# Kernel optimization log

Hardware: AMD Instinct MI355X
Metric: run time of the kernel (lower is better)

The kernel has to match this reference:

```python
import jax, jax.numpy as jnp
import numpy as np

CONTACT_THRESH = 0.01
COLLISION_THRESH = 0.005
WEIGHT_PEN = 100.0
WEIGHT_MISS = 10.0
# MANO fingertip + palm contact-zone vertex indices (hardcoded in module)
CONTACT_IDX = np.array([745, 317, 444, 556, 673, 95, 182, 234, 279, 320])

SCALE = 0.1  # place points in a 0.1 m cube so mm-scale thresholds are meaningful


def setup_inputs() -> dict:
    key = jax.random.key(0)
    k1, k2, k3, k4 = jax.random.split(key, 4)
    B, NH, V = 8, 778, 40000
    hand_verts = jax.random.uniform(k1, (B, NH, 3), dtype=jnp.float32) * SCALE
    obj_verts = jax.random.uniform(k2, (B, V, 3), dtype=jnp.float32) * SCALE
    hand_faces = jax.random.randint(k3, (1538, 3), 0, NH, dtype=jnp.int64 if jax.config.read('jax_enable_x64') else jnp.int32)
    obj_faces = jax.random.randint(k4, (79996, 3), 0, V, dtype=jnp.int64 if jax.config.read('jax_enable_x64') else jnp.int32)
    return {"hand_verts": hand_verts, "obj_verts": obj_verts,
            "hand_faces": hand_faces, "obj_faces": obj_faces}


def _min_dists(a, b):
    """Brute-force 1-NN: min Euclidean distance from each point in a [B,N,3] to b [B,M,3] -> [B,N]."""
    a_sq = jnp.sum(a * a, axis=-1, keepdims=True)          # [B,N,1]
    b_sq = jnp.sum(b * b, axis=-1)                          # [B,M]
    ab = jnp.einsum('bnd,bmd->bnm', a, b)                   # [B,N,M]
    d2 = jnp.maximum(a_sq + b_sq[:, None, :] - 2.0 * ab, 0.0)
    return jnp.sqrt(jnp.min(d2, axis=2))                    # [B,N]


def _masked_mean(vals, mask):
    cnt = jnp.sum(mask)
    s = jnp.sum(jnp.where(mask, vals, 0.0))
    return jnp.where(cnt > 0, s / jnp.maximum(cnt, 1).astype(vals.dtype), jnp.zeros((), vals.dtype))


def reference(hand_verts, obj_verts, hand_faces, obj_faces):
    # faces are unused by the loss (as in the torch module)
    idx = jnp.asarray(CONTACT_IDX)
    # distances are computed under no_grad / detached in the original
    dists = jax.lax.stop_gradient(_min_dists(hand_verts, obj_verts))              # [B,778]
    contact_dists = jax.lax.stop_gradient(_min_dists(hand_verts[:, idx, :], obj_verts))  # [B,10]

    pen_mask = dists < COLLISION_THRESH
    pen_loss = _masked_mean((COLLISION_THRESH - dists) ** 2, pen_mask)

    att_mask = (contact_dists > COLLISION_THRESH) & (contact_dists < CONTACT_THRESH)
    att_loss = _masked_mean(contact_dists ** 2, att_mask)

    contact_loss = WEIGHT_PEN * pen_loss + WEIGHT_MISS * att_loss
    dist_mean = jnp.mean(dists)
    num_contacts = jnp.sum(att_mask).astype(jnp.int32)
    num_penetrations = jnp.sum(pen_mask).astype(jnp.int32)
    return (contact_loss, pen_loss, att_loss, dist_mean, num_contacts, num_penetrations)
```

## Files before the change

kernel.cpp:

```cpp
#include <hip/hip_runtime.h>
#include <math.h>

constexpr int NH     = 778;
constexpr int T      = 16;
constexpr int NTILES = (NH + T - 1) / T;
constexpr int NHPAD  = NTILES * T;
constexpr int BLK    = 256;
constexpr int CHUNKP = 2560;
constexpr int LPP    = CHUNKP / BLK;

__global__ __launch_bounds__(256) void transform_kernel(
    const float* __restrict__ hand,
    const float* __restrict__ obj,
    float4* __restrict__ otf,
    float4* __restrict__ htf,
    unsigned int* __restrict__ minb,
    int V, int Vpad, int B)
{
    const int i = blockIdx.x * 256 + threadIdx.x;
    if (i < B * NH) minb[i] = 0x7F7F7F7Fu;
    if (i < B * NHPAD) {
        const int b = i / NHPAD;
        const int h = min(i - b * NHPAD, NH - 1);
        const float* p = hand + ((size_t)b * NH + h) * 3;
        const float x = p[0], y = p[1], z = p[2];
        htf[i] = make_float4(-2.f * x, -2.f * y, -2.f * z,
                             fmaf(x, x, fmaf(y, y, z * z)));
    }
    if (i < B * Vpad) {
        const int b = i / Vpad;
        const int j = i - b * Vpad;
        if (j < V) {
            const float* p = obj + ((size_t)b * V + j) * 3;
            const float x = p[0], y = p[1], z = p[2];
            otf[i] = make_float4(x, y, z, fmaf(x, x, fmaf(y, y, z * z)));
        } else {
            otf[i] = make_float4(0.f, 0.f, 0.f, 3.4e38f);
        }
    }
}

__global__ __launch_bounds__(BLK, 4) void nn_min_kernel(
    const float4* __restrict__ otf,
    const float4* __restrict__ htf,
    unsigned int* __restrict__ minb,
    int Vpad)
{
    const int tile = blockIdx.x;
    const int c    = blockIdx.y;
    const int b    = blockIdx.z;
    const int tid  = threadIdx.x;

    const float4* hp = htf + (size_t)b * NHPAD + tile * T;
    float4 h[T];
#pragma unroll
    for (int t = 0; t < T; ++t) h[t] = hp[t];

    const float4* op = otf + (size_t)b * Vpad + c * CHUNKP + tid;
    float m[T];
#pragma unroll
    for (int t = 0; t < T; ++t) m[t] = 3.4e38f;

#pragma unroll
    for (int k = 0; k < LPP; ++k) {
        const float4 o = op[k * BLK];
#pragma unroll
        for (int t = 0; t < T; ++t) {
            float v = fmaf(h[t].x, o.x, o.w);
            v = fmaf(h[t].y, o.y, v);
            v = fmaf(h[t].z, o.z, v);
            m[t] = fminf(m[t], v);
        }
    }

#pragma unroll
    for (int t = 0; t < T; ++t) {
        float v = m[t] + h[t].w;
#pragma unroll
        for (int d = 1; d < 64; d <<= 1)
            v = fminf(v, __shfl_xor(v, d));
        m[t] = v;
    }

    __shared__ float red[4][T];
    const int wave = tid >> 6;
    const int lane = tid & 63;
    if (lane == 0) {
#pragma unroll
        for (int t = 0; t < T; ++t) red[wave][t] = m[t];
    }
    __syncthreads();

    if (tid < T) {
        const float v = fminf(fminf(red[0][tid], red[1][tid]),
                              fminf(red[2][tid], red[3][tid]));
        const int hidx = tile * T + tid;
        if (hidx < NH) {
            const unsigned bits = __float_as_uint(fmaxf(v, 0.f));
            unsigned int* p = &minb[b * NH + hidx];
            if (bits < *((volatile unsigned int*)p)) atomicMin(p, bits);
        }
    }
}

constexpr int FBLK = 256, FSLOT = 3, FCHUNK = 157;
__global__ __launch_bounds__(FBLK) void nn_min_raw_kernel(
    const float* __restrict__ hand, const float* __restrict__ obj,
    unsigned int* __restrict__ minb, int V)
{
    const int b = blockIdx.y, c = blockIdx.x, tid = threadIdx.x;
    const int j0 = c * FCHUNK;
    const int cnt = min(FCHUNK, V - j0);
    const float* op = obj + ((size_t)b * V + j0) * 3;
    const float* hb = hand + (size_t)b * NH * 3;
    float hx[FSLOT], hy[FSLOT], hz[FSLOT], m[FSLOT];
#pragma unroll
    for (int s = 0; s < FSLOT; ++s) {
        const int h = tid + s * FBLK;
        hx[s] = hb[h * 3 + 0]; hy[s] = hb[h * 3 + 1]; hz[s] = hb[h * 3 + 2];
        m[s] = 3.4e38f;
    }
#pragma unroll 2
    for (int j = 0; j < cnt; ++j) {
        const float ox = op[3 * j + 0], oy = op[3 * j + 1], oz = op[3 * j + 2];
#pragma unroll
        for (int s = 0; s < FSLOT; ++s) {
            const float dx = ox - hx[s], dy = oy - hy[s], dz = oz - hz[s];
            m[s] = fminf(m[s], fmaf(dx, dx, fmaf(dy, dy, dz * dz)));
        }
    }
#pragma unroll
    for (int s = 0; s < FSLOT; ++s) {
        const int h = tid + s * FBLK;
        const unsigned bits = __float_as_uint(fmaxf(m[s], 0.f));
        unsigned int* p = &minb[b * NH + h];
        if (bits < *((volatile unsigned int*)p)) atomicMin(p, bits);
    }
    if (tid < NH - FSLOT * FBLK) {
        const int h = FSLOT * FBLK + tid;
        const float tx = hb[h * 3 + 0], ty = hb[h * 3 + 1], tz = hb[h * 3 + 2];
        float tm = 3.4e38f;
        for (int j = 0; j < cnt; ++j) {
            const float dx = op[3 * j + 0] - tx;
            const float dy = op[3 * j + 1] - ty;
            const float dz = op[3 * j + 2] - tz;
            tm = fminf(tm, fmaf(dx, dx, fmaf(dy, dy, dz * dz)));
        }
        unsigned int* p = &minb[b * NH + h];
        const unsigned bits = __float_as_uint(fmaxf(tm, 0.f));
        if (bits < *((volatile unsigned int*)p)) atomicMin(p, bits);
    }
}

__global__ __launch_bounds__(256) void finalize_kernel(
    const unsigned int* __restrict__ minb, float* __restrict__ out, int B)
{
    constexpr float COLL = 0.005f;
    constexpr float CONT = 0.01f;
    const int total = B * NH;
    const int tid = threadIdx.x;

    double sum_d = 0.0, pen_sum = 0.0, att_sum = 0.0;
    int pen_cnt = 0, att_cnt = 0;
    for (int i = tid; i < total; i += 256) {
        const float d = sqrtf(__uint_as_float(minb[i]));
        sum_d += (double)d;
        if (d < COLL) { const float t = COLL - d; pen_sum += (double)(t * t); pen_cnt++; }
        const int n = i % NH;
        const bool isc = (n == 745) | (n == 317) | (n == 444) | (n == 556) |
                         (n == 673) | (n == 95)  | (n == 182) | (n == 234) |
                         (n == 279) | (n == 320);
        if (isc & (d > COLL) & (d < CONT)) { att_sum += (double)(d * d); att_cnt++; }
    }

    __shared__ double sd[256], sp[256], sa[256];
    __shared__ int    cp[256], ca[256];
    sd[tid] = sum_d; sp[tid] = pen_sum; sa[tid] = att_sum;
    cp[tid] = pen_cnt; ca[tid] = att_cnt;
    __syncthreads();
    for (int off = 128; off > 0; off >>= 1) {
        if (tid < off) {
            sd[tid] += sd[tid + off]; sp[tid] += sp[tid + off];
            sa[tid] += sa[tid + off];
            cp[tid] += cp[tid + off]; ca[tid] += ca[tid + off];
        }
        __syncthreads();
    }
    if (tid == 0) {
        const double pen_loss = cp[0] > 0 ? sp[0] / (double)cp[0] : 0.0;
        const double att_loss = ca[0] > 0 ? sa[0] / (double)ca[0] : 0.0;
        out[0] = (float)(100.0 * pen_loss + 10.0 * att_loss);
        out[1] = (float)pen_loss;
        out[2] = (float)att_loss;
        out[3] = (float)(sd[0] / (double)total);
        out[4] = (float)ca[0];
        out[5] = (float)cp[0];
    }
}

extern "C" void kernel_launch(void* const* d_in, const int* in_sizes, int n_in,
                              void* d_out, int out_size, void* d_ws, size_t ws_size,
                              hipStream_t stream) {
    const float* hand = (const float*)d_in[0];
    const float* obj  = (const float*)d_in[1];

    const int B = in_sizes[0] / (NH * 3);
    const int V = in_sizes[1] / (B * 3);
    const int nchunks = (V + CHUNKP - 1) / CHUNKP;
    const int Vpad = nchunks * CHUNKP;

    unsigned int* minb = (unsigned int*)d_ws;
    float4* htf = (float4*)((char*)d_ws + 65536);
    float4* otf = (float4*)((char*)d_ws + 65536 + 131072);
    const size_t need = 65536 + 131072 + (size_t)B * Vpad * sizeof(float4);

    if (ws_size >= need) {
        const int tot = B * Vpad;
        transform_kernel<<<(tot + 255) / 256, 256, 0, stream>>>(
            hand, obj, otf, htf, minb, V, Vpad, B);
        dim3 grid(NTILES, nchunks, B);
        nn_min_kernel<<<grid, BLK, 0, stream>>>(otf, htf, minb, Vpad);
    } else {
        hipMemsetAsync(d_ws, 0x7F, (size_t)B * NH * sizeof(unsigned int), stream);
        dim3 grid((V + FCHUNK - 1) / FCHUNK, B);
        nn_min_raw_kernel<<<grid, FBLK, 0, stream>>>(hand, obj, minb, V);
    }
    finalize_kernel<<<1, 256, 0, stream>>>(minb, (float*)d_out, B);
}
```

Measured before the change: 109.3 us.

## Reuse register-held object points across four hand tiles per block with LDS transpose reduction

Each block now loads its chunk of object points into registers once and loops over four groups of 16 hand vertices, so object data is reused across more hand vertices and the grid shrinks from 49 to 13 blocks in x. The per-vertex 64-lane shuffle reduction is replaced by a padded shared-memory transpose, where each lane mins 16 values, followed by two shuffles. It also drops the cross-wave __syncthreads and has each wave issue its own atomics. This cuts global loads and shuffle overhead, at the cost of more registers (occupancy hint lowered to 3), about 16KB of LDS per block, and four times more atomics.

```diff
diff --git a/kernel.cpp b/kernel.cpp
--- a/kernel.cpp
+++ b/kernel.cpp
@@ -3,8 +3,9 @@
 
 constexpr int NH     = 778;
 constexpr int T      = 16;
-constexpr int NTILES = (NH + T - 1) / T;
-constexpr int NHPAD  = NTILES * T;
+constexpr int G      = 4;
+constexpr int NBX    = 13;
+constexpr int NHPAD  = NBX * G * T;
 constexpr int BLK    = 256;
 constexpr int CHUNKP = 2560;
 constexpr int LPP    = CHUNKP / BLK;
@@ -40,65 +41,71 @@
     }
 }
 
-__global__ __launch_bounds__(BLK, 4) void nn_min_kernel(
+__global__ __launch_bounds__(BLK, 3) void nn_min_kernel(
     const float4* __restrict__ otf,
     const float4* __restrict__ htf,
     unsigned int* __restrict__ minb,
     int Vpad)
 {
-    const int tile = blockIdx.x;
-    const int c    = blockIdx.y;
-    const int b    = blockIdx.z;
-    const int tid  = threadIdx.x;
-
-    const float4* hp = htf + (size_t)b * NHPAD + tile * T;
-    float4 h[T];
-#pragma unroll
-    for (int t = 0; t < T; ++t) h[t] = hp[t];
-
-    const float4* op = otf + (size_t)b * Vpad + c * CHUNKP + tid;
-    float m[T];
-#pragma unroll
-    for (int t = 0; t < T; ++t) m[t] = 3.4e38f;
-
-#pragma unroll
-    for (int k = 0; k < LPP; ++k) {
-        const float4 o = op[k * BLK];
-#pragma unroll
-        for (int t = 0; t < T; ++t) {
-            float v = fmaf(h[t].x, o.x, o.w);
-            v = fmaf(h[t].y, o.y, v);
-            v = fmaf(h[t].z, o.z, v);
-            m[t] = fminf(m[t], v);
-        }
-    }
-
-#pragma unroll
-    for (int t = 0; t < T; ++t) {
-        float v = m[t] + h[t].w;
-#pragma unroll
-        for (int d = 1; d < 64; d <<= 1)
-            v = fminf(v, __shfl_xor(v, d));
-        m[t] = v;
-    }
-
-    __shared__ float red[4][T];
+    __shared__ float s_red[4][16 * 65];
+    const int bx  = blockIdx.x;
+    const int c   = blockIdx.y;
+    const int b   = blockIdx.z;
+    const int tid = threadIdx.x;
     const int wave = tid >> 6;
     const int lane = tid & 63;
-    if (lane == 0) {
-#pragma unroll
-        for (int t = 0; t < T; ++t) red[wave][t] = m[t];
-    }
-    __syncthreads();
-
-    if (tid < T) {
-        const float v = fminf(fminf(red[0][tid], red[1][tid]),
-                              fminf(red[2][tid], red[3][tid]));
-        const int hidx = tile * T + tid;
-        if (hidx < NH) {
-            const unsigned bits = __float_as_uint(fmaxf(v, 0.f));
-            unsigned int* p = &minb[b * NH + hidx];
-            if (bits < *((volatile unsigned int*)p)) atomicMin(p, bits);
+
+    const float4* op = otf + (size_t)b * Vpad + c * CHUNKP + tid;
+    float4 o[LPP];
+#pragma unroll
+    for (int k = 0; k < LPP; ++k) o[k] = op[k * BLK];
+
+    const float4* hp = htf + (size_t)b * NHPAD + bx * (G * T);
+    float* sw = &s_red[wave][0];
+    const int r   = lane & 15;
+    const int seg = lane >> 4;
+
+#pragma unroll
+    for (int g = 0; g < G; ++g) {
+        float4 h[T];
+#pragma unroll
+        for (int t = 0; t < T; ++t) h[t] = hp[g * T + t];
+
+        float m[T];
+#pragma unroll
+        for (int t = 0; t < T; ++t) m[t] = 3.4e38f;
+
+#pragma unroll
+        for (int k = 0; k < LPP; ++k) {
+#pragma unroll
+            for (int t = 0; t < T; ++t) {
+                float v = fmaf(h[t].x, o[k].x, o[k].w);
+                v = fmaf(h[t].y, o[k].y, v);
+                v = fmaf(h[t].z, o[k].z, v);
+                m[t] = fminf(m[t], v);
+            }
+        }
+
+#pragma unroll
+        for (int t = 0; t < T; ++t) sw[t * 65 + lane] = m[t] + h[t].w;
+        __builtin_amdgcn_wave_barrier();
+
+        float v = 3.4e38f;
+        const int base = r * 65 + seg * 16;
+#pragma unroll
+        for (int j = 0; j < 16; ++j) v = fminf(v, sw[base + j]);
+        __builtin_amdgcn_wave_barrier();
+
+        v = fminf(v, __shfl_xor(v, 16));
+        v = fminf(v, __shfl_xor(v, 32));
+
+        if (seg == 0) {
+            const int hidx = (bx * G + g) * T + r;
+            if (hidx < NH) {
+                const unsigned bits = __float_as_uint(fmaxf(v, 0.f));
+                unsigned int* p = &minb[b * NH + hidx];
+                if (bits < *((volatile unsigned int*)p)) atomicMin(p, bits);
+            }
         }
     }
 }
@@ -218,7 +225,7 @@
         const int tot = B * Vpad;
         transform_kernel<<<(tot + 255) / 256, 256, 0, stream>>>(
             hand, obj, otf, htf, minb, V, Vpad, B);
-        dim3 grid(NTILES, nchunks, B);
+        dim3 grid(NBX, nchunks, B);
         nn_min_kernel<<<grid, BLK, 0, stream>>>(otf, htf, minb, Vpad);
     } else {
         hipMemsetAsync(d_ws, 0x7F, (size_t)B * NH * sizeof(unsigned int), stream);
```

After: 109.6 us. Within noise of the previous version (+0.2%).
